# Optimization experiments

Hardware: AMD Instinct MI355X
Metric: run time of the kernel (lower is better)

The kernel has to match this reference:

```python
import jax, jax.numpy as jnp
import numpy as np

B, T, F = 64, 512, 256
ENC = 256      # encoder output dim
P = 128        # projection_dim
H = 256        # gru_hidden_dim
K = 12         # num_future_steps
TEMP = 0.1


def setup_inputs() -> dict:
    key = jax.random.key(0)
    ks = jax.random.split(key, 12)
    s = lambda *d: 1.0 / np.sqrt(d[0])
    return {
        "x_seq": jax.random.normal(ks[0], (B, T, F), jnp.float32),
        # encoder: Dense(F -> ENC)
        "W_enc": jax.random.normal(ks[1], (F, ENC), jnp.float32) * s(F),
        "b_enc": jnp.zeros((ENC,), jnp.float32),
        # projection: Dense(ENC -> P)
        "W_proj": jax.random.normal(ks[2], (ENC, P), jnp.float32) * s(ENC),
        "b_proj": jnp.zeros((P,), jnp.float32),
        # GRUCell (flax convention: input dense has bias, hidden dense bias only on n)
        "Wi": jax.random.normal(ks[3], (P, 3 * H), jnp.float32) * s(P),
        "bi": jnp.zeros((3 * H,), jnp.float32),
        "Wh": jax.random.normal(ks[4], (H, 3 * H), jnp.float32) * s(H),
        "bhn": jnp.zeros((H,), jnp.float32),
        # K predictors: Dense(H -> P)
        "Wp": jax.random.normal(ks[5], (K, H, P), jnp.float32) * s(H),
        "bp": jnp.zeros((K, P), jnp.float32),
    }


def _gru_scan(z_seq, Wi, bi, Wh, bhn):
    # z_seq: [B, T, P] -> c_seq: [B, T, H]
    def step(h, x_t):
        gi = x_t @ Wi + bi          # [B, 3H]
        gh = h @ Wh                 # [B, 3H]
        ir, iz, inn = jnp.split(gi, 3, axis=-1)
        hr, hz, hn = jnp.split(gh, 3, axis=-1)
        r = jax.nn.sigmoid(ir + hr)
        z = jax.nn.sigmoid(iz + hz)
        n = jnp.tanh(inn + r * (hn + bhn))
        h_new = (1.0 - z) * n + z * h
        return h_new, h_new

    h0 = jnp.zeros((z_seq.shape[0], Wh.shape[0]), z_seq.dtype)
    _, c = jax.lax.scan(step, h0, jnp.swapaxes(z_seq, 0, 1))  # c: [T, B, H]
    return jnp.swapaxes(c, 0, 1)


def reference(x_seq, W_enc, b_enc, W_proj, b_proj, Wi, bi, Wh, bhn, Wp, bp):
    # encoder per timestep (vmap(vmap(Dense)) == batched matmul)
    z_seq = x_seq @ W_enc + b_enc                 # [B, T, ENC]
    z_seq = z_seq @ W_proj + b_proj               # [B, T, P]
    c_seq = _gru_scan(z_seq, Wi, bi, Wh, bhn)     # [B, T, H]

    Tlen = z_seq.shape[1]
    loss = jnp.asarray(0.0, z_seq.dtype)
    for k in range(1, K + 1):
        if Tlen - k <= 0:
            continue
        z_pos = z_seq[:, k:]                      # [B, T-k, P]
        pred = c_seq[:, :-k] @ Wp[k - 1] + bp[k - 1]  # [B, T-k, P]
        logits = jnp.einsum('btd,bkd->btk', pred, z_pos) / TEMP
        labels = jnp.arange(logits.shape[1])
        # NOTE: faithful to source: [..., labels] with labels=arange is an
        # identity gather along the last axis (not a diagonal pick).
        loss = loss + jnp.mean(-jax.nn.log_softmax(logits, axis=-1)[..., labels])
    return loss / K
```

## Files before the change

kernel.cpp:

```cpp
#include <hip/hip_runtime.h>
#include <hip/hip_bf16.h>
#include <math.h>

#define B_   64
#define T_   512
#define F_   256
#define ENC_ 256
#define P_   128
#define H_   256
#define K_   12
#define INV_TEMP 10.0f

typedef unsigned short u16;
typedef _Float16 half2v __attribute__((ext_vector_type(2)));
union U2H { unsigned int u; half2v h; };
typedef __attribute__((ext_vector_type(8))) short bf16x8;
typedef __attribute__((ext_vector_type(4))) float f32x4;
union BF8 { bf16x8 v; u16 e[8]; };

__device__ __forceinline__ float dot2f16(unsigned int a, unsigned int b, float c) {
    U2H ua; ua.u = a; U2H ub; ub.u = b;
#if __has_builtin(__builtin_amdgcn_fdot2)
    return __builtin_amdgcn_fdot2(ua.h, ub.h, c, false);
#else
    return fmaf((float)ua.h.x, (float)ub.h.x, fmaf((float)ua.h.y, (float)ub.h.y, c));
#endif
}
__device__ __forceinline__ float rcpf(float x) {
#if __has_builtin(__builtin_amdgcn_rcpf)
    return __builtin_amdgcn_rcpf(x);
#else
    return 1.f / x;
#endif
}
__device__ __forceinline__ u16 f2bf(float f) {
    unsigned int u = __float_as_uint(f);
    unsigned int r = (u + 0x7fffu + ((u >> 16) & 1u)) >> 16;
    return (u16)r;
}
__device__ __forceinline__ float bf2f(u16 v) {
    return __uint_as_float(((unsigned int)v) << 16);
}
__device__ __forceinline__ float bflo(unsigned int u) { return __uint_as_float(u << 16); }
__device__ __forceinline__ float bfhi(unsigned int u) { return __uint_as_float(u & 0xffff0000u); }
__device__ __forceinline__ float wave_sum(float v) {
    #pragma unroll
    for (int o = 32; o > 0; o >>= 1) v += __shfl_down(v, o, 64);
    return v;
}

__global__ __launch_bounds__(256) void setup_conv(const float* __restrict__ Wh,
                                                  uint2* __restrict__ Whh,
                                                  const float* __restrict__ Wi,
                                                  u16* __restrict__ Wit,
                                                  const float* __restrict__ Wp,
                                                  u16* __restrict__ Wpt,
                                                  const float* __restrict__ We,
                                                  const float* __restrict__ be,
                                                  const float* __restrict__ Wpj,
                                                  const float* __restrict__ bpj,
                                                  u16* __restrict__ Wct,
                                                  float* __restrict__ bc,
                                                  float* __restrict__ accum) {
    int bid = blockIdx.x;
    if (bid < 192) {
        int idx = bid * 256 + threadIdx.x;
        int i4 = idx / 768, j = idx % 768;
        U2H lo, hi;
        lo.h.x = (_Float16)Wh[(size_t)(4 * i4 + 0) * 768 + j];
        lo.h.y = (_Float16)Wh[(size_t)(4 * i4 + 1) * 768 + j];
        hi.h.x = (_Float16)Wh[(size_t)(4 * i4 + 2) * 768 + j];
        hi.h.y = (_Float16)Wh[(size_t)(4 * i4 + 3) * 768 + j];
        Whh[idx] = make_uint2(lo.u, hi.u);
    } else if (bid < 288) {
        __shared__ float tile[32][33];
        int b2 = bid - 192;
        int n0 = (b2 % 24) * 32, k0 = (b2 / 24) * 32;
        int tx = threadIdx.x & 31, ty = threadIdx.x >> 5;
        #pragma unroll
        for (int i = 0; i < 32; i += 8)
            tile[ty + i][tx] = Wi[(size_t)(k0 + ty + i) * 768 + n0 + tx];
        __syncthreads();
        #pragma unroll
        for (int i = 0; i < 32; i += 8)
            Wit[(size_t)(n0 + ty + i) * 128 + k0 + tx] = f2bf(tile[tx][ty + i]);
    } else if (bid < 672) {
        __shared__ float tile2[32][33];
        int b3 = bid - 288;
        int kq = b3 / 32, rem = b3 % 32;
        int h0 = (rem % 8) * 32, p0 = (rem / 8) * 32;
        int tx = threadIdx.x & 31, ty = threadIdx.x >> 5;
        #pragma unroll
        for (int i = 0; i < 32; i += 8)
            tile2[ty + i][tx] = Wp[(size_t)kq * H_ * P_ + (size_t)(h0 + ty + i) * P_ + p0 + tx];
        __syncthreads();
        #pragma unroll
        for (int i = 0; i < 32; i += 8)
            Wpt[(size_t)kq * P_ * H_ + (size_t)(p0 + ty + i) * H_ + h0 + tx] = f2bf(tile2[tx][ty + i]);
    } else {
        int f = (bid - 672) * 2 + (threadIdx.x >> 7);
        int p = threadIdx.x & 127;
        if (f < F_) {
            float a = 0.f;
            for (int e = 0; e < ENC_; e++) a = fmaf(We[f * ENC_ + e], Wpj[e * P_ + p], a);
            Wct[(size_t)p * F_ + f] = f2bf(a);
        } else if (f == F_) {
            float a = bpj[p];
            for (int e = 0; e < ENC_; e++) a = fmaf(be[e], Wpj[e * P_ + p], a);
            bc[p] = a;
        } else {
            #pragma unroll
            for (int i = 0; i < 8; i++) accum[p * 8 + i] = 0.f;
        }
    }
}

__global__ __launch_bounds__(256) void gemm_mfma_f32a(const float* __restrict__ A,
                                                      const u16* __restrict__ Bt,
                                                      const float* __restrict__ bias,
                                                      u16* __restrict__ Ch,
                                                      int N, int K) {
    int tid  = threadIdx.x;
    int w    = tid >> 6;
    int lane = tid & 63;
    int col  = lane & 15;
    int quad = lane >> 4;
    int bm = blockIdx.y * 64, bn = blockIdx.x * 128;

    f32x4 acc[8] = {};
    const float* arow = A + (size_t)(bm + w * 16 + col) * K;
    #pragma unroll
    for (int k0 = 0; k0 < K; k0 += 32) {
        float4 v0 = *(const float4*)(arow + k0 + quad * 8);
        float4 v1 = *(const float4*)(arow + k0 + quad * 8 + 4);
        BF8 af;
        af.e[0] = f2bf(v0.x); af.e[1] = f2bf(v0.y); af.e[2] = f2bf(v0.z); af.e[3] = f2bf(v0.w);
        af.e[4] = f2bf(v1.x); af.e[5] = f2bf(v1.y); af.e[6] = f2bf(v1.z); af.e[7] = f2bf(v1.w);
        #pragma unroll
        for (int nt = 0; nt < 8; nt++) {
            bf16x8 bf = *(const bf16x8*)(Bt + (size_t)(bn + nt * 16 + col) * K + k0 + quad * 8);
            acc[nt] = __builtin_amdgcn_mfma_f32_16x16x32_bf16(af.v, bf, acc[nt], 0, 0, 0);
        }
    }
    #pragma unroll
    for (int nt = 0; nt < 8; nt++) {
        int gn = bn + nt * 16 + col;
        float bv = bias[gn];
        #pragma unroll
        for (int r = 0; r < 4; r++) {
            int gm = bm + w * 16 + quad * 4 + r;
            Ch[(size_t)gm * N + gn] = f2bf(acc[nt][r] + bv);
        }
    }
}

__global__ __launch_bounds__(256) void gemm_mfma(const u16* __restrict__ A,
                                                 const u16* __restrict__ Bt,
                                                 const float* __restrict__ bias,
                                                 u16* __restrict__ Ch,
                                                 int N, int K) {
    int tid  = threadIdx.x;
    int w    = tid >> 6;
    int lane = tid & 63;
    int col  = lane & 15;
    int quad = lane >> 4;
    int bm = blockIdx.y * 64, bn = blockIdx.x * 128;

    f32x4 acc[8] = {};
    const u16* arow = A + (size_t)(bm + w * 16 + col) * K;
    #pragma unroll
    for (int k0 = 0; k0 < K; k0 += 32) {
        bf16x8 af = *(const bf16x8*)(arow + k0 + quad * 8);
        #pragma unroll
        for (int nt = 0; nt < 8; nt++) {
            bf16x8 bf = *(const bf16x8*)(Bt + (size_t)(bn + nt * 16 + col) * K + k0 + quad * 8);
            acc[nt] = __builtin_amdgcn_mfma_f32_16x16x32_bf16(af, bf, acc[nt], 0, 0, 0);
        }
    }
    #pragma unroll
    for (int nt = 0; nt < 8; nt++) {
        int gn = bn + nt * 16 + col;
        float bv = bias[gn];
        #pragma unroll
        for (int r = 0; r < 4; r++) {
            int gm = bm + w * 16 + quad * 4 + r;
            Ch[(size_t)gm * N + gn] = f2bf(acc[nt][r] + bv);
        }
    }
}

__global__ __attribute__((amdgpu_flat_work_group_size(512, 512), amdgpu_waves_per_eu(2, 2)))
void gru_zsum_kernel(const u16* __restrict__ gi,
                     const uint2* __restrict__ Whh,
                     const float* __restrict__ bhn,
                     u16* __restrict__ ch,
                     const u16* __restrict__ zh,
                     float* __restrict__ zsum) {
    __shared__ __align__(16) char shraw[8704];
    int tid = threadIdx.x;

    if (blockIdx.x >= B_) {
        float (*part)[128] = (float(*)[128])shraw;
        int b   = blockIdx.x - B_;
        int pg  = tid & 31;
        int g   = tid >> 5;
        const u16* zb = zh + (size_t)b * T_ * P_;
        float s0 = 0.f, s1 = 0.f, s2 = 0.f, s3 = 0.f;
        for (int t = 1 + g; t < T_; t += 16) {
            uint2 v = *(const uint2*)(zb + (size_t)t * P_ + pg * 4);
            s0 += bflo(v.x); s1 += bfhi(v.x);
            s2 += bflo(v.y); s3 += bfhi(v.y);
        }
        part[g][pg * 4 + 0] = s0; part[g][pg * 4 + 1] = s1;
        part[g][pg * 4 + 2] = s2; part[g][pg * 4 + 3] = s3;
        __syncthreads();
        if (tid < 128) {
            float s = 0.f;
            #pragma unroll
            for (int g2 = 0; g2 < 16; g2++) s += part[g2][tid];
            zsum[(size_t)b * P_ + tid] = s;
        }
        return;
    }

    _Float16* hbuf = (_Float16*)shraw;
    float4 (*ps)[256] = (float4(*)[256])(shraw + 512);
    int b    = blockIdx.x;
    int j    = tid & 255;
    int half = tid >> 8;

    uint2 wR[32], wZ[32], wN[32];
    {
        const uint2* base = Whh + (size_t)(half * 32) * 768;
        const uint2* cR = base + j;
        const uint2* cZ = base + 256 + j;
        const uint2* cN = base + 512 + j;
        #pragma unroll
        for (int i = 0; i < 32; i++) {
            wR[i] = cR[(size_t)i * 768];
            wZ[i] = cZ[(size_t)i * 768];
            wN[i] = cN[(size_t)i * 768];
        }
        #pragma unroll
        for (int i = 0; i < 32; i++) {
            asm volatile("" : "+v"(wR[i].x), "+v"(wR[i].y));
            asm volatile("" : "+v"(wZ[i].x), "+v"(wZ[i].y));
            asm volatile("" : "+v"(wN[i].x), "+v"(wN[i].y));
        }
    }
    if (tid < H_) hbuf[tid] = (_Float16)0.f;
    float bh = bhn[j];
    float hloc = 0.f;

    const u16* gib = gi + (size_t)b * T_ * 768;
    u16* cb = ch + (size_t)b * T_ * H_;
    float ir = 0.f, iz = 0.f, inn = 0.f;
    if (tid < 256) { ir = bf2f(gib[j]); iz = bf2f(gib[256 + j]); inn = bf2f(gib[512 + j]); }
    __syncthreads();

    const uint2* hw = (const uint2*)hbuf;
    #pragma unroll 1
    for (int t = 0; t < T_; t++) {
        float nir = 0.f, niz = 0.f, ninn = 0.f;
        if (tid < 256) {
            int tn = (t + 1 < T_) ? t + 1 : t;
            const u16* gtn = gib + (size_t)tn * 768;
            nir = bf2f(gtn[j]); niz = bf2f(gtn[256 + j]); ninn = bf2f(gtn[512 + j]);
        }
        float ar0 = 0.f, ar1 = 0.f, az0 = 0.f, az1 = 0.f, an0 = 0.f, an1 = 0.f;
        #pragma unroll
        for (int i = 0; i < 32; i++) {
            uint2 hv = hw[half * 32 + i];
            ar0 = dot2f16(hv.x, wR[i].x, ar0);
            ar1 = dot2f16(hv.y, wR[i].y, ar1);
            az0 = dot2f16(hv.x, wZ[i].x, az0);
            az1 = dot2f16(hv.y, wZ[i].y, az1);
            an0 = dot2f16(hv.x, wN[i].x, an0);
            an1 = dot2f16(hv.y, wN[i].y, an1);
        }
        ps[half][j] = make_float4(ar0 + ar1, az0 + az1, an0 + an1, 0.f);
        __syncthreads();
        if (tid < 256) {
            float4 p0 = ps[0][j], p1 = ps[1][j];
            float ar = p0.x + p1.x;
            float az = p0.y + p1.y;
            float an = p0.z + p1.z;
            float r   = rcpf(1.f + __expf(-(ir + ar)));
            float zg  = rcpf(1.f + __expf(-(iz + az)));
            float xn  = inn + r * (an + bh);
            float n   = fmaf(2.f, rcpf(1.f + __expf(-2.f * xn)), -1.f);
            hloc = (1.f - zg) * n + zg * hloc;
            cb[(size_t)t * H_ + j] = f2bf(hloc);
            hbuf[j] = (_Float16)hloc;
        }
        ir = nir; iz = niz; inn = ninn;
        __syncthreads();
    }
}

__global__ __launch_bounds__(512) void loss_fused(const u16* __restrict__ ch,
                                                  const u16* __restrict__ Wpt,
                                                  const float* __restrict__ bp,
                                                  const u16* __restrict__ zh,
                                                  const float* __restrict__ zsum,
                                                  float* __restrict__ accum) {
    __shared__ u16 Pst[128][136];
    __shared__ u16 Zt[64][136];
    __shared__ float sS[128];
    __shared__ float red[8];
    int k  = blockIdx.z + 1;
    int b  = blockIdx.y;
    int t0 = blockIdx.x * 128;
    int Tk = T_ - k;
    int tid  = threadIdx.x;
    int w    = tid >> 6;
    int lane = tid & 63;
    int col  = lane & 15;
    int quad = lane >> 4;
    const u16* zb = zh + (size_t)b * T_ * P_;

    if (tid < 128) {
        float s = zsum[(size_t)b * P_ + tid];
        for (int t = 1; t < k; t++) s -= bf2f(zb[(size_t)t * P_ + tid]);
        sS[tid] = s;
    }

    {
        f32x4 acc[8] = {};
        const u16* arow = ch + ((size_t)b * T_ + t0 + w * 16 + col) * H_;
        const u16* wk   = Wpt + (size_t)(k - 1) * P_ * H_;
        #pragma unroll
        for (int k0 = 0; k0 < 8; k0++) {
            bf16x8 af = *(const bf16x8*)(arow + k0 * 32 + quad * 8);
            #pragma unroll
            for (int nt = 0; nt < 8; nt++) {
                bf16x8 bf = *(const bf16x8*)(wk + (size_t)(nt * 16 + col) * H_ + k0 * 32 + quad * 8);
                acc[nt] = __builtin_amdgcn_mfma_f32_16x16x32_bf16(af, bf, acc[nt], 0, 0, 0);
            }
        }
        #pragma unroll
        for (int nt = 0; nt < 8; nt++) {
            float bias = bp[(size_t)(k - 1) * P_ + nt * 16 + col];
            #pragma unroll
            for (int r = 0; r < 4; r++)
                Pst[w * 16 + quad * 4 + r][nt * 16 + col] = f2bf(acc[nt][r] + bias);
        }
    }
    __syncthreads();

    float mloc[4], sloc[4];
    #pragma unroll
    for (int r = 0; r < 4; r++) { mloc[r] = -INFINITY; sloc[r] = 0.f; }

    for (int ct = 0; ct < Tk; ct += 64) {
        __syncthreads();
        {
            int c = tid;
            #pragma unroll
            for (int rep = 0; rep < 2; rep++, c += 512) {
                int row = c >> 4;
                int off = (c & 15) * 8;
                int tcol = k + ct + row;
                *(uint4*)&Zt[row][off] = *(const uint4*)(zb + (size_t)tcol * P_ + off);
            }
        }
        __syncthreads();
        f32x4 acc[4] = {};
        #pragma unroll
        for (int k0 = 0; k0 < 4; k0++) {
            bf16x8 af = *(const bf16x8*)(&Pst[w * 16 + col][k0 * 32 + quad * 8]);
            #pragma unroll
            for (int nt = 0; nt < 4; nt++) {
                bf16x8 bf = *(const bf16x8*)(&Zt[nt * 16 + col][k0 * 32 + quad * 8]);
                acc[nt] = __builtin_amdgcn_mfma_f32_16x16x32_bf16(af, bf, acc[nt], 0, 0, 0);
            }
        }
        #pragma unroll
        for (int r = 0; r < 4; r++) {
            float l[4];
            float tmax = -INFINITY;
            #pragma unroll
            for (int nt = 0; nt < 4; nt++) {
                bool valid = (ct + nt * 16 + col) < Tk;
                l[nt] = valid ? acc[nt][r] * INV_TEMP : -INFINITY;
                tmax = fmaxf(tmax, l[nt]);
            }
            float mnew = fmaxf(mloc[r], tmax);
            float e = __expf(l[0] - mnew) + __expf(l[1] - mnew)
                    + __expf(l[2] - mnew) + __expf(l[3] - mnew);
            sloc[r] = sloc[r] * __expf(mloc[r] - mnew) + e;
            mloc[r] = mnew;
        }
    }
    #pragma unroll
    for (int r = 0; r < 4; r++) {
        #pragma unroll
        for (int o = 1; o < 16; o <<= 1) {
            float mo = __shfl_xor(mloc[r], o, 64);
            float so = __shfl_xor(sloc[r], o, 64);
            float mn = fmaxf(mloc[r], mo);
            sloc[r] = sloc[r] * __expf(mloc[r] - mn) + so * __expf(mo - mn);
            mloc[r] = mn;
        }
    }
    float tkinv = INV_TEMP / (float)Tk;
    float scale = 1.0f / ((float)K_ * (float)B_ * (float)Tk);
    float bs = 0.f;
    #pragma unroll
    for (int r = 0; r < 4; r++) {
        int row = w * 16 + quad * 4 + r;
        BF8 pv;
        pv.v = *(const bf16x8*)(&Pst[row][col * 8]);
        float d = 0.f;
        #pragma unroll
        for (int m = 0; m < 8; m++) d = fmaf(bf2f(pv.e[m]), sS[col * 8 + m], d);
        #pragma unroll
        for (int o = 1; o < 16; o <<= 1) d += __shfl_xor(d, o, 64);
        int gr = t0 + row;
        if (gr < Tk) bs += mloc[r] + __logf(sloc[r]) - d * tkinv;
    }
    if (col != 0) bs = 0.f;
    bs = wave_sum(bs);
    if (lane == 0) red[w] = bs;
    __syncthreads();
    if (tid == 0) {
        float tot = 0.f;
        #pragma unroll
        for (int i = 0; i < 8; i++) tot += red[i];
        atomicAdd(&accum[(blockIdx.x * 809 + b * 67 + blockIdx.z * 131) & 1023],
                  tot * scale);
    }
}

__global__ void finalize(const float* __restrict__ accum, float* __restrict__ out) {
    int tid = threadIdx.x;
    __shared__ float red[4];
    float v = 0.f;
    for (int i = tid; i < 1024; i += 256) v += accum[i];
    float sres = wave_sum(v);
    if ((tid & 63) == 0) red[tid >> 6] = sres;
    __syncthreads();
    if (tid == 0) out[0] = red[0] + red[1] + red[2] + red[3];
}

extern "C" void kernel_launch(void* const* d_in, const int* in_sizes, int n_in,
                              void* d_out, int out_size, void* d_ws, size_t ws_size,
                              hipStream_t stream) {
    const float* x      = (const float*)d_in[0];
    const float* W_enc  = (const float*)d_in[1];
    const float* b_enc  = (const float*)d_in[2];
    const float* W_proj = (const float*)d_in[3];
    const float* b_proj = (const float*)d_in[4];
    const float* Wi     = (const float*)d_in[5];
    const float* bi     = (const float*)d_in[6];
    const float* Wh     = (const float*)d_in[7];
    const float* bhn    = (const float*)d_in[8];
    const float* Wp     = (const float*)d_in[9];
    const float* bp     = (const float*)d_in[10];
    float* out = (float*)d_out;

    float* ws    = (float*)d_ws;
    float* bc    = ws;
    float* accum = bc + 128;
    uint2* Whh   = (uint2*)(ws + 1152);
    u16* Wct     = (u16*)(ws + 99456);
    u16* Wit     = (u16*)(ws + 115840);
    u16* Wpt     = (u16*)(ws + 164992);
    u16* zh      = (u16*)(ws + 361600);
    float* zsum  = ws + 2458752;
    u16* gi      = (u16*)(ws + 2466944);
    u16* ch      = (u16*)(ws + 15049856);

    const int MT = B_ * T_;

    setup_conv<<<801, 256, 0, stream>>>(Wh, Whh, Wi, Wit, Wp, Wpt,
                                        W_enc, b_enc, W_proj, b_proj, Wct, bc, accum);
    gemm_mfma_f32a<<<dim3(1, MT / 64), 256, 0, stream>>>(x, Wct, bc, zh, P_, F_);
    gemm_mfma<<<dim3(6, MT / 64), 256, 0, stream>>>(zh, Wit, bi, gi, 3 * H_, P_);
    gru_zsum_kernel<<<2 * B_, 512, 0, stream>>>(gi, Whh, bhn, ch, zh, zsum);
    loss_fused<<<dim3(4, B_, K_), 512, 0, stream>>>(ch, Wpt, bp, zh, zsum, accum);
    finalize<<<1, 256, 0, stream>>>(accum, out);
}
```

Measured before the change: 1.057 ms.

## Run GRU recurrence on FP8 MFMA with register-resident quantized Wh, 8 batches per block

Adds a GRU kernel in which each block handles 8 batch rows and computes h@Wh with fp8×bf8 MFMA instructions. Wh is quantized to bf8 (e5m2) in setup and kept entirely in registers, and the hidden state is quantized to fp8 (e4m3) in double-buffered shared memory. This replaces the earlier one-batch-per-block fp16 dot2 recurrence, aiming to cut per-step latency and the number of blocks serialized on the time loop. The cost is lower precision in the recurrent matmul, which can drift over 512 steps, plus extra setup work to quantize Wh.

```diff
diff --git a/kernel.cpp b/kernel.cpp
--- a/kernel.cpp
+++ b/kernel.cpp
@@ -18,6 +18,12 @@
 typedef __attribute__((ext_vector_type(4))) float f32x4;
 union BF8 { bf16x8 v; u16 e[8]; };
 
+#if defined(__has_builtin)
+#if __has_builtin(__builtin_amdgcn_mfma_f32_16x16x32_fp8_bf8)
+#define HAVE_FP8MFMA 1
+#endif
+#endif
+
 __device__ __forceinline__ float dot2f16(unsigned int a, unsigned int b, float c) {
     U2H ua; ua.u = a; U2H ub; ub.u = b;
 #if __has_builtin(__builtin_amdgcn_fdot2)
@@ -43,10 +49,44 @@
 }
 __device__ __forceinline__ float bflo(unsigned int u) { return __uint_as_float(u << 16); }
 __device__ __forceinline__ float bfhi(unsigned int u) { return __uint_as_float(u & 0xffff0000u); }
+__device__ __forceinline__ unsigned f2e5(float f) {
+    U2H c; c.h.x = (_Float16)f; c.h.y = (_Float16)0.f;
+    unsigned h = c.u & 0xFFFFu;
+    return ((h + 0x7Fu + ((h >> 8) & 1u)) >> 8) & 0xFFu;
+}
+__device__ __forceinline__ unsigned f2e4(float f) {
+#if __has_builtin(__builtin_amdgcn_cvt_pk_fp8_f32)
+    return (unsigned)__builtin_amdgcn_cvt_pk_fp8_f32(f, f, 0, false) & 0xFFu;
+#else
+    unsigned u = __float_as_uint(f);
+    unsigned s = (u >> 24) & 0x80u;
+    int e = (int)((u >> 23) & 0xFF) - 127;
+    unsigned m = u & 0x7FFFFFu;
+    if (e >= 9) return s | 0x7Eu;
+    if (e >= -6) {
+        unsigned mant = m >> 20, rest = m & 0xFFFFFu;
+        if (rest > 0x80000u || (rest == 0x80000u && (mant & 1u))) mant++;
+        unsigned v = ((unsigned)(e + 7) << 3) + mant;
+        if (v > 0x7Eu) v = 0x7Eu;
+        return s | v;
+    }
+    if (e < -10) return s;
+    unsigned full = 0x800000u | m;
+    int shift = 20 + (-6 - e);
+    unsigned mant = full >> shift;
+    unsigned rem = full & ((1u << shift) - 1u);
+    unsigned half = 1u << (shift - 1);
+    if (rem > half || (rem == half && (mant & 1u))) mant++;
+    return s | mant;
+#endif
+}
 __device__ __forceinline__ float wave_sum(float v) {
     #pragma unroll
     for (int o = 32; o > 0; o >>= 1) v += __shfl_down(v, o, 64);
     return v;
+}
+__device__ __forceinline__ int wtile(int wv, int s) {
+    return (s < 2) ? (2 * wv + s) : (s < 4) ? (16 + 2 * wv + s - 2) : (32 + 2 * wv + s - 4);
 }
 
 __global__ __launch_bounds__(256) void setup_conv(const float* __restrict__ Wh,
@@ -61,7 +101,8 @@
                                                   const float* __restrict__ bpj,
                                                   u16* __restrict__ Wct,
                                                   float* __restrict__ bc,
-                                                  float* __restrict__ accum) {
+                                                  float* __restrict__ accum,
+                                                  uint2* __restrict__ Wq) {
     int bid = blockIdx.x;
     if (bid < 192) {
         int idx = bid * 256 + threadIdx.x;
@@ -97,7 +138,7 @@
         #pragma unroll
         for (int i = 0; i < 32; i += 8)
             Wpt[(size_t)kq * P_ * H_ + (size_t)(p0 + ty + i) * H_ + h0 + tx] = f2bf(tile2[tx][ty + i]);
-    } else {
+    } else if (bid < 801) {
         int f = (bid - 672) * 2 + (threadIdx.x >> 7);
         int p = threadIdx.x & 127;
         if (f < F_) {
@@ -112,6 +153,23 @@
             #pragma unroll
             for (int i = 0; i < 8; i++) accum[p * 8 + i] = 0.f;
         }
+    } else {
+        int idx = (bid - 801) * 256 + threadIdx.x;
+        int lane = idx & 63;
+        int rest = idx >> 6;
+        int k0 = rest & 7;
+        int s  = (rest >> 3) % 6;
+        int wv = rest / 48;
+        int col  = wtile(wv, s) * 16 + (lane & 15);
+        int kh0  = k0 * 32 + (lane >> 4) * 8;
+        unsigned lo = 0, hi = 0;
+        #pragma unroll
+        for (int j = 0; j < 4; j++)
+            lo |= f2e5(Wh[(size_t)(kh0 + j) * 768 + col]) << (8 * j);
+        #pragma unroll
+        for (int j = 0; j < 4; j++)
+            hi |= f2e5(Wh[(size_t)(kh0 + 4 + j) * 768 + col]) << (8 * j);
+        Wq[idx] = make_uint2(lo, hi);
     }
 }
 
@@ -188,6 +246,131 @@
         }
     }
 }
+
+#ifdef HAVE_FP8MFMA
+__global__ __attribute__((amdgpu_flat_work_group_size(512, 512), amdgpu_waves_per_eu(2, 2)))
+void gru_zsum_mfma(const u16* __restrict__ gi,
+                   const long long* __restrict__ Wq,
+                   const float* __restrict__ bhn,
+                   u16* __restrict__ ch,
+                   const u16* __restrict__ zh,
+                   float* __restrict__ zsum) {
+    __shared__ __align__(16) char shraw[8704];
+    int tid = threadIdx.x;
+
+    if (blockIdx.x >= 8) {
+        float (*part)[128] = (float(*)[128])shraw;
+        int b   = blockIdx.x - 8;
+        int pg  = tid & 31;
+        int g   = tid >> 5;
+        const u16* zb = zh + (size_t)b * T_ * P_;
+        float s0 = 0.f, s1 = 0.f, s2 = 0.f, s3 = 0.f;
+        for (int t = 1 + g; t < T_; t += 16) {
+            uint2 v = *(const uint2*)(zb + (size_t)t * P_ + pg * 4);
+            s0 += bflo(v.x); s1 += bfhi(v.x);
+            s2 += bflo(v.y); s3 += bfhi(v.y);
+        }
+        part[g][pg * 4 + 0] = s0; part[g][pg * 4 + 1] = s1;
+        part[g][pg * 4 + 2] = s2; part[g][pg * 4 + 3] = s3;
+        __syncthreads();
+        if (tid < 128) {
+            float s = 0.f;
+            #pragma unroll
+            for (int g2 = 0; g2 < 16; g2++) s += part[g2][tid];
+            zsum[(size_t)b * P_ + tid] = s;
+        }
+        return;
+    }
+
+    char (*hA)[16 * 264] = (char(*)[16 * 264])shraw;
+    int wv   = tid >> 6;
+    int lane = tid & 63;
+    int c    = lane & 15;
+    int quad = lane >> 4;
+
+    long long wq[48];
+    {
+        const long long* wp = Wq + (size_t)wv * 48 * 64 + lane;
+        #pragma unroll
+        for (int i = 0; i < 48; i++) wq[i] = wp[(size_t)i * 64];
+        #pragma unroll
+        for (int i = 0; i < 48; i++) asm volatile("" : "+v"(wq[i]));
+    }
+    for (int i = tid; i < 2 * 16 * 264 / 4; i += 512) ((unsigned*)shraw)[i] = 0u;
+
+    int jc0 = (2 * wv + 0) * 16 + c;
+    int jc1 = (2 * wv + 1) * 16 + c;
+    float bh0 = bhn[jc0], bh1 = bhn[jc1];
+
+    float hl[8];
+    #pragma unroll
+    for (int q = 0; q < 8; q++) hl[q] = 0.f;
+
+    float pir[8], piz[8], pin[8];
+    bool gact = quad < 2;
+    int bg0 = blockIdx.x * 8 + quad * 4;
+    if (gact) {
+        #pragma unroll
+        for (int r = 0; r < 4; r++) {
+            const u16* gp = gi + ((size_t)(bg0 + r) * T_) * 768;
+            pir[r]     = bf2f(gp[jc0]); piz[r]     = bf2f(gp[256 + jc0]); pin[r]     = bf2f(gp[512 + jc0]);
+            pir[4 + r] = bf2f(gp[jc1]); piz[4 + r] = bf2f(gp[256 + jc1]); pin[4 + r] = bf2f(gp[512 + jc1]);
+        }
+    }
+    __syncthreads();
+
+    int cur = 0;
+    #pragma unroll 1
+    for (int t = 0; t < T_; t++) {
+        f32x4 acc[6] = {};
+        const char* hrow = hA[cur] + (size_t)c * 264 + quad * 8;
+        #pragma unroll
+        for (int k0 = 0; k0 < 8; k0++) {
+            long long av = *(const long long*)(hrow + k0 * 32);
+            #pragma unroll
+            for (int s = 0; s < 6; s++)
+                acc[s] = __builtin_amdgcn_mfma_f32_16x16x32_fp8_bf8(av, wq[s * 8 + k0], acc[s], 0, 0, 0);
+        }
+        float nir[8], niz[8], nin[8];
+        if (gact) {
+            int tn = (t + 1 < T_) ? t + 1 : t;
+            #pragma unroll
+            for (int r = 0; r < 4; r++) {
+                const u16* gp = gi + ((size_t)(bg0 + r) * T_ + tn) * 768;
+                nir[r]     = bf2f(gp[jc0]); niz[r]     = bf2f(gp[256 + jc0]); nin[r]     = bf2f(gp[512 + jc0]);
+                nir[4 + r] = bf2f(gp[jc1]); niz[4 + r] = bf2f(gp[256 + jc1]); nin[4 + r] = bf2f(gp[512 + jc1]);
+            }
+        }
+        if (gact) {
+            char* hnxt = hA[cur ^ 1];
+            #pragma unroll
+            for (int d = 0; d < 2; d++) {
+                int jc = d ? jc1 : jc0;
+                float bh = d ? bh1 : bh0;
+                #pragma unroll
+                for (int r = 0; r < 4; r++) {
+                    int q = d * 4 + r;
+                    float gr = acc[d][r], gz = acc[2 + d][r], gn = acc[4 + d][r];
+                    float rr = rcpf(1.f + __expf(-(pir[q] + gr)));
+                    float zz = rcpf(1.f + __expf(-(piz[q] + gz)));
+                    float xn = pin[q] + rr * (gn + bh);
+                    float nn = fmaf(2.f, rcpf(1.f + __expf(-2.f * xn)), -1.f);
+                    float h  = fmaf(zz, hl[q] - nn, nn);
+                    hl[q] = h;
+                    ch[((size_t)(bg0 + r) * T_ + t) * H_ + jc] = f2bf(h);
+                    hnxt[(size_t)(quad * 4 + r) * 264 + jc] = (char)f2e4(h);
+                }
+            }
+        }
+        __syncthreads();
+        cur ^= 1;
+        if (gact) {
+            #pragma unroll
+            for (int q = 0; q < 8; q++) { pir[q] = nir[q]; piz[q] = niz[q]; pin[q] = nin[q]; }
+        }
+    }
+}
+#endif
 
 __global__ __attribute__((amdgpu_flat_work_group_size(512, 512), amdgpu_waves_per_eu(2, 2)))
 void gru_zsum_kernel(const u16* __restrict__ gi,
@@ -355,11 +538,11 @@
     for (int ct = 0; ct < Tk; ct += 64) {
         __syncthreads();
         {
-            int c = tid;
-            #pragma unroll
-            for (int rep = 0; rep < 2; rep++, c += 512) {
-                int row = c >> 4;
-                int off = (c & 15) * 8;
+            int cc = tid;
+            #pragma unroll
+            for (int rep = 0; rep < 2; rep++, cc += 512) {
+                int row = cc >> 4;
+                int off = (cc & 15) * 8;
                 int tcol = k + ct + row;
                 *(uint4*)&Zt[row][off] = *(const uint4*)(zb + (size_t)tcol * P_ + off);
             }
@@ -470,14 +653,20 @@
     float* zsum  = ws + 2458752;
     u16* gi      = (u16*)(ws + 2466944);
     u16* ch      = (u16*)(ws + 15049856);
+    uint2* Wq    = (uint2*)(ws + 19244160);
 
     const int MT = B_ * T_;
 
-    setup_conv<<<801, 256, 0, stream>>>(Wh, Whh, Wi, Wit, Wp, Wpt,
-                                        W_enc, b_enc, W_proj, b_proj, Wct, bc, accum);
+    setup_conv<<<897, 256, 0, stream>>>(Wh, Whh, Wi, Wit, Wp, Wpt,
+                                        W_enc, b_enc, W_proj, b_proj, Wct, bc, accum,
+                                        Wq);
     gemm_mfma_f32a<<<dim3(1, MT / 64), 256, 0, stream>>>(x, Wct, bc, zh, P_, F_);
     gemm_mfma<<<dim3(6, MT / 64), 256, 0, stream>>>(zh, Wit, bi, gi, 3 * H_, P_);
+#ifdef HAVE_FP8MFMA
+    gru_zsum_mfma<<<8 + B_, 512, 0, stream>>>(gi, (const long long*)Wq, bhn, ch, zh, zsum);
+#else
     gru_zsum_kernel<<<2 * B_, 512, 0, stream>>>(gi, Whh, bhn, ch, zh, zsum);
+#endif
     loss_fused<<<dim3(4, B_, K_), 512, 0, stream>>>(ch, Wpt, bp, zh, zsum, accum);
     finalize<<<1, 256, 0, stream>>>(accum, out);
 }
```

Result: no change. 1.054 ms (-0.2%).
